# Kernel optimization log

Measured on AMD Instinct MI355X. Metric: run time of the kernel, lower is better.

The kernel has to match this reference:

```python
import jax, jax.numpy as jnp
import numpy as np


def setup_inputs() -> dict:
    key = jax.random.key(0)
    k1, k2, k3 = jax.random.split(key, 3)
    B, T, D = 64, 256, 512
    real = jax.random.normal(k1, (B, T, D), dtype=jnp.float32)
    imag = jax.random.normal(k2, (B, T, D), dtype=jnp.float32)
    weight = jax.random.uniform(k3, (B, T, 1), dtype=jnp.float32)
    return {"real": real, "imag": imag, "weight": weight}


def reference(real, imag, weight):
    # Weighted complex outer-product mixture:
    #   out_r[b] = sum_t w[b,t] * (r_t r_t^T + i_t i_t^T)
    #   out_i[b] = sum_t w[b,t] * (i_t r_t^T - r_t i_t^T)
    # Equivalent to the original per-sample loop + TxDxD outer products,
    # but fused: scale one operand by w and contract over t directly.
    w = weight[..., 0]  # [B, T]
    rw = real * w[..., None]  # [B, T, D]
    iw = imag * w[..., None]
    out_r = jnp.einsum('btd,bte->bde', rw, real) + jnp.einsum('btd,bte->bde', iw, imag)
    out_i = jnp.einsum('btd,bte->bde', iw, real) - jnp.einsum('btd,bte->bde', rw, imag)
    return (out_r, out_i)
```

## Files before the change

kernel.cpp:

```cpp
#include <hip/hip_runtime.h>
#include <cstdint>
#include <cstddef>

#define BB 64
#define TT 256
#define DD 512
#define BK 32
#define TILEM 128

typedef short bf16x8 __attribute__((ext_vector_type(8)));
typedef float f32x4  __attribute__((ext_vector_type(4)));

typedef __attribute__((address_space(1))) const void* gptr_t;
typedef __attribute__((address_space(3))) void* sptr_t;

static __device__ __forceinline__ unsigned short f2bf(float x) {
  unsigned u = __builtin_bit_cast(unsigned, x) + 0x8000u;
  return (unsigned short)(u >> 16);
}

__global__ __launch_bounds__(256, 2)
void ComplexMixture_54838142435828_kernel(const float* __restrict__ re,
                                          const float* __restrict__ im,
                                          const float* __restrict__ wt,
                                          float* __restrict__ out) {
  __shared__ __attribute__((aligned(16))) float sT[4 * BK * 128];
  __shared__ float sw[TT];

  const int tid = threadIdx.x;

  const int L = blockIdx.x;
  const int c = L & 7;
  const int s = L >> 3;
  const int b  = c * 8 + (s >> 4);
  const int t5 = s & 15;
  const int d0 = (t5 >> 2) * TILEM;
  const int e0 = (t5 & 3) * TILEM;

  sw[tid] = wt[b * TT + tid];

  const int lane = tid & 63;
  const int wid  = tid >> 6;
  const int wm = (wid >> 1) * 64;
  const int wn = (wid & 1) * 64;
  const int quad = lane >> 4;
  const int l16  = lane & 15;

  const int scol = (wid & 2) ? e0 : d0;
  const float* sbase = (wid & 1) ? im : re;
  const int ksub  = lane >> 5;
  const int dloc4 = (lane & 31) * 4;

  f32x4 accR[4][4], accI[4][4];
  #pragma unroll
  for (int mt = 0; mt < 4; ++mt)
    #pragma unroll
    for (int nt = 0; nt < 4; ++nt) {
      accR[mt][nt] = (f32x4){0.f, 0.f, 0.f, 0.f};
      accI[mt][nt] = (f32x4){0.f, 0.f, 0.f, 0.f};
    }

  for (int kt = 0; kt < TT; kt += BK) {
    __syncthreads();

    const float* gsrc = sbase + ((size_t)(b * TT + kt + ksub)) * DD + scol + dloc4;
    float* lbase = &sT[wid * (BK * 128)];
    #pragma unroll
    for (int p = 0; p < 16; ++p) {
      __builtin_amdgcn_global_load_lds((gptr_t)(const void*)(gsrc + (size_t)(2 * p) * DD),
                                       (sptr_t)(void*)(lbase + p * 256),
                                       16, 0, 0);
    }
    __syncthreads();

    float wv[8];
    #pragma unroll
    for (int j = 0; j < 8; ++j) wv[j] = sw[kt + quad * 8 + j];

    bf16x8 bR[4], bI[4];
    #pragma unroll
    for (int nt = 0; nt < 4; ++nt) {
      const int dl = wn + nt * 16 + l16;
      union { unsigned short h[8]; bf16x8 v; } ur, ui;
      #pragma unroll
      for (int j = 0; j < 8; ++j) {
        ur.h[j] = f2bf(sT[2 * (BK * 128) + (quad * 8 + j) * 128 + dl]);
        ui.h[j] = f2bf(sT[3 * (BK * 128) + (quad * 8 + j) * 128 + dl]);
      }
      bR[nt] = ur.v;
      bI[nt] = ui.v;
    }

    #pragma unroll
    for (int mt = 0; mt < 4; ++mt) {
      const int dl = wm + mt * 16 + l16;
      union { unsigned short h[8]; bf16x8 v; } ur, ui;
      #pragma unroll
      for (int j = 0; j < 8; ++j) {
        const float r = sT[0 * (BK * 128) + (quad * 8 + j) * 128 + dl] * wv[j];
        const float i = sT[1 * (BK * 128) + (quad * 8 + j) * 128 + dl] * wv[j];
        ur.h[j] = f2bf(r);
        ui.h[j] = f2bf(i);
      }
      const bf16x8 aR = ur.v;
      const bf16x8 aI = ui.v;
      const bf16x8 aRn = aR ^ (bf16x8)((short)0x8000);
      #pragma unroll
      for (int nt = 0; nt < 4; ++nt) {
        accR[mt][nt] = __builtin_amdgcn_mfma_f32_16x16x32_bf16(aR,  bR[nt], accR[mt][nt], 0, 0, 0);
        accR[mt][nt] = __builtin_amdgcn_mfma_f32_16x16x32_bf16(aI,  bI[nt], accR[mt][nt], 0, 0, 0);
        accI[mt][nt] = __builtin_amdgcn_mfma_f32_16x16x32_bf16(aI,  bR[nt], accI[mt][nt], 0, 0, 0);
        accI[mt][nt] = __builtin_amdgcn_mfma_f32_16x16x32_bf16(aRn, bI[nt], accI[mt][nt], 0, 0, 0);
      }
    }
  }

  const size_t NOFF = (size_t)BB * DD * DD;
  #pragma unroll
  for (int mt = 0; mt < 4; ++mt) {
    #pragma unroll
    for (int r = 0; r < 4; ++r) {
      const int drow = d0 + wm + mt * 16 + quad * 4 + r;
      const size_t rowOff = ((size_t)(b * DD + drow)) * DD;
      #pragma unroll
      for (int nt = 0; nt < 4; ++nt) {
        const int ecol = e0 + wn + nt * 16 + l16;
        out[rowOff + ecol]        = accR[mt][nt][r];
        out[NOFF + rowOff + ecol] = accI[mt][nt][r];
      }
    }
  }
}

extern "C" void kernel_launch(void* const* d_in, const int* in_sizes, int n_in,
                              void* d_out, int out_size, void* d_ws, size_t ws_size,
                              hipStream_t stream) {
  const float* re = (const float*)d_in[0];
  const float* im = (const float*)d_in[1];
  const float* wt = (const float*)d_in[2];
  float* out = (float*)d_out;
  ComplexMixture_54838142435828_kernel<<<dim3(1024), dim3(256), 0, stream>>>(re, im, wt, out);
}
```

Before: 225.8 us.

## Exploit Hermitian symmetry, switch to 32x32 MFMA and double-buffer LDS staging

Uses the symmetry out_r^T = out_r and out_i^T = -out_i to compute only the 10 upper-triangular 128x128 tiles per batch. Off-diagonal tiles write their mirror through an LDS transpose. Also switches to 32x32x16 bf16 MFMA with BK=16 and double-buffers the global-to-LDS staging so the next chunk loads while the current one computes. This removes roughly 37.5% of the MFMA and load work. In exchange it adds extra transposed stores, more syncs, and an uneven grid of 640 blocks.

```diff
diff --git a/kernel.cpp b/kernel.cpp
--- a/kernel.cpp
+++ b/kernel.cpp
@@ -5,11 +5,12 @@
 #define BB 64
 #define TT 256
 #define DD 512
-#define BK 32
+#define BK 16
 #define TILEM 128
 
 typedef short bf16x8 __attribute__((ext_vector_type(8)));
-typedef float f32x4  __attribute__((ext_vector_type(4)));
+typedef float f32x16 __attribute__((ext_vector_type(16)));
+typedef float f32x4v __attribute__((ext_vector_type(4)));
 
 typedef __attribute__((address_space(1))) const void* gptr_t;
 typedef __attribute__((address_space(3))) void* sptr_t;
@@ -19,23 +20,22 @@
   return (unsigned short)(u >> 16);
 }
 
+#define STG(buf, t, idx) sB[(buf) * 8192 + (t) * 2048 + (idx)]
+
 __global__ __launch_bounds__(256, 2)
 void ComplexMixture_54838142435828_kernel(const float* __restrict__ re,
                                           const float* __restrict__ im,
                                           const float* __restrict__ wt,
                                           float* __restrict__ out) {
-  __shared__ __attribute__((aligned(16))) float sT[4 * BK * 128];
+  __shared__ __attribute__((aligned(16))) float sB[16896];
   __shared__ float sw[TT];
 
   const int tid = threadIdx.x;
-
-  const int L = blockIdx.x;
-  const int c = L & 7;
-  const int s = L >> 3;
-  const int b  = c * 8 + (s >> 4);
-  const int t5 = s & 15;
-  const int d0 = (t5 >> 2) * TILEM;
-  const int e0 = (t5 & 3) * TILEM;
+  const int b = blockIdx.y;
+  static const int TIa[10] = {0, 1, 1, 2, 2, 2, 3, 3, 3, 3};
+  static const int TJa[10] = {0, 0, 1, 0, 1, 2, 0, 1, 2, 3};
+  const int d0 = TIa[blockIdx.x] * TILEM;
+  const int e0 = TJa[blockIdx.x] * TILEM;
 
   sw[tid] = wt[b * TT + tid];
 
@@ -43,90 +43,120 @@
   const int wid  = tid >> 6;
   const int wm = (wid >> 1) * 64;
   const int wn = (wid & 1) * 64;
-  const int quad = lane >> 4;
-  const int l16  = lane & 15;
+  const int kh  = lane >> 5;
+  const int l32 = lane & 31;
 
+  const float* sbase = (wid & 1) ? im : re;
   const int scol = (wid & 2) ? e0 : d0;
-  const float* sbase = (wid & 1) ? im : re;
-  const int ksub  = lane >> 5;
-  const int dloc4 = (lane & 31) * 4;
+  const int dl4  = l32 * 4;
 
-  f32x4 accR[4][4], accI[4][4];
+  f32x16 accR[2][2], accI[2][2];
   #pragma unroll
-  for (int mt = 0; mt < 4; ++mt)
+  for (int mt = 0; mt < 2; ++mt)
     #pragma unroll
-    for (int nt = 0; nt < 4; ++nt) {
-      accR[mt][nt] = (f32x4){0.f, 0.f, 0.f, 0.f};
-      accI[mt][nt] = (f32x4){0.f, 0.f, 0.f, 0.f};
+    for (int nt = 0; nt < 2; ++nt) {
+      #pragma unroll
+      for (int r = 0; r < 16; ++r) { accR[mt][nt][r] = 0.f; accI[mt][nt][r] = 0.f; }
     }
 
-  for (int kt = 0; kt < TT; kt += BK) {
+  auto stage = [&](int it, int buf) {
+    const float* g = sbase + ((size_t)(b * TT + it * BK + kh)) * DD + scol + dl4;
+    const int lb = buf * 8192 + wid * 2048;
+    #pragma unroll
+    for (int p = 0; p < 8; ++p) {
+      __builtin_amdgcn_global_load_lds((gptr_t)(const void*)(g + (size_t)(2 * p) * DD),
+                                       (sptr_t)(void*)&sB[lb + p * 256], 16, 0, 0);
+    }
+  };
+
+  stage(0, 0);
+
+  for (int it = 0; it < TT / BK; ++it) {
     __syncthreads();
-
-    const float* gsrc = sbase + ((size_t)(b * TT + kt + ksub)) * DD + scol + dloc4;
-    float* lbase = &sT[wid * (BK * 128)];
-    #pragma unroll
-    for (int p = 0; p < 16; ++p) {
-      __builtin_amdgcn_global_load_lds((gptr_t)(const void*)(gsrc + (size_t)(2 * p) * DD),
-                                       (sptr_t)(void*)(lbase + p * 256),
-                                       16, 0, 0);
-    }
-    __syncthreads();
+    if (it < TT / BK - 1) stage(it + 1, (it + 1) & 1);
+    const int buf = it & 1;
 
     float wv[8];
     #pragma unroll
-    for (int j = 0; j < 8; ++j) wv[j] = sw[kt + quad * 8 + j];
+    for (int j = 0; j < 8; ++j) wv[j] = sw[it * BK + kh * 8 + j];
 
-    bf16x8 bR[4], bI[4];
+    bf16x8 aR[2], aI[2], bR[2], bI[2];
     #pragma unroll
-    for (int nt = 0; nt < 4; ++nt) {
-      const int dl = wn + nt * 16 + l16;
+    for (int mt = 0; mt < 2; ++mt) {
+      const int m = wm + mt * 32 + l32;
       union { unsigned short h[8]; bf16x8 v; } ur, ui;
       #pragma unroll
       for (int j = 0; j < 8; ++j) {
-        ur.h[j] = f2bf(sT[2 * (BK * 128) + (quad * 8 + j) * 128 + dl]);
-        ui.h[j] = f2bf(sT[3 * (BK * 128) + (quad * 8 + j) * 128 + dl]);
+        const int idx = (kh * 8 + j) * 128 + m;
+        ur.h[j] = f2bf(STG(buf, 0, idx) * wv[j]);
+        ui.h[j] = f2bf(STG(buf, 1, idx) * wv[j]);
       }
-      bR[nt] = ur.v;
-      bI[nt] = ui.v;
+      aR[mt] = ur.v; aI[mt] = ui.v;
+    }
+    #pragma unroll
+    for (int nt = 0; nt < 2; ++nt) {
+      const int n = wn + nt * 32 + l32;
+      union { unsigned short h[8]; bf16x8 v; } ur, ui;
+      #pragma unroll
+      for (int j = 0; j < 8; ++j) {
+        const int idx = (kh * 8 + j) * 128 + n;
+        ur.h[j] = f2bf(STG(buf, 2, idx));
+        ui.h[j] = f2bf(STG(buf, 3, idx));
+      }
+      bR[nt] = ur.v; bI[nt] = ui.v;
     }
 
     #pragma unroll
-    for (int mt = 0; mt < 4; ++mt) {
-      const int dl = wm + mt * 16 + l16;
-      union { unsigned short h[8]; bf16x8 v; } ur, ui;
+    for (int mt = 0; mt < 2; ++mt) {
+      const bf16x8 aRn = aR[mt] ^ (bf16x8)((short)0x8000);
       #pragma unroll
-      for (int j = 0; j < 8; ++j) {
-        const float r = sT[0 * (BK * 128) + (quad * 8 + j) * 128 + dl] * wv[j];
-        const float i = sT[1 * (BK * 128) + (quad * 8 + j) * 128 + dl] * wv[j];
-        ur.h[j] = f2bf(r);
-        ui.h[j] = f2bf(i);
-      }
-      const bf16x8 aR = ur.v;
-      const bf16x8 aI = ui.v;
-      const bf16x8 aRn = aR ^ (bf16x8)((short)0x8000);
-      #pragma unroll
-      for (int nt = 0; nt < 4; ++nt) {
-        accR[mt][nt] = __builtin_amdgcn_mfma_f32_16x16x32_bf16(aR,  bR[nt], accR[mt][nt], 0, 0, 0);
-        accR[mt][nt] = __builtin_amdgcn_mfma_f32_16x16x32_bf16(aI,  bI[nt], accR[mt][nt], 0, 0, 0);
-        accI[mt][nt] = __builtin_amdgcn_mfma_f32_16x16x32_bf16(aI,  bR[nt], accI[mt][nt], 0, 0, 0);
-        accI[mt][nt] = __builtin_amdgcn_mfma_f32_16x16x32_bf16(aRn, bI[nt], accI[mt][nt], 0, 0, 0);
+      for (int nt = 0; nt < 2; ++nt) {
+        accR[mt][nt] = __builtin_amdgcn_mfma_f32_32x32x16_bf16(aR[mt], bR[nt], accR[mt][nt], 0, 0, 0);
+        accR[mt][nt] = __builtin_amdgcn_mfma_f32_32x32x16_bf16(aI[mt], bI[nt], accR[mt][nt], 0, 0, 0);
+        accI[mt][nt] = __builtin_amdgcn_mfma_f32_32x32x16_bf16(aI[mt], bR[nt], accI[mt][nt], 0, 0, 0);
+        accI[mt][nt] = __builtin_amdgcn_mfma_f32_32x32x16_bf16(aRn,    bI[nt], accI[mt][nt], 0, 0, 0);
       }
     }
   }
 
   const size_t NOFF = (size_t)BB * DD * DD;
   #pragma unroll
-  for (int mt = 0; mt < 4; ++mt) {
+  for (int mt = 0; mt < 2; ++mt) {
     #pragma unroll
-    for (int r = 0; r < 4; ++r) {
-      const int drow = d0 + wm + mt * 16 + quad * 4 + r;
-      const size_t rowOff = ((size_t)(b * DD + drow)) * DD;
+    for (int r = 0; r < 16; ++r) {
+      const int row_l = (r & 3) + 8 * (r >> 2) + 4 * kh;
+      const size_t rowOff = ((size_t)(b * DD + d0 + wm + mt * 32 + row_l)) * DD;
       #pragma unroll
-      for (int nt = 0; nt < 4; ++nt) {
-        const int ecol = e0 + wn + nt * 16 + l16;
-        out[rowOff + ecol]        = accR[mt][nt][r];
-        out[NOFF + rowOff + ecol] = accI[mt][nt][r];
+      for (int nt = 0; nt < 2; ++nt) {
+        const int col = e0 + wn + nt * 32 + l32;
+        out[rowOff + col]        = accR[mt][nt][r];
+        out[NOFF + rowOff + col] = accI[mt][nt][r];
+      }
+    }
+  }
+
+  if (d0 != e0) {
+    #pragma unroll
+    for (int pass = 0; pass < 2; ++pass) {
+      __syncthreads();
+      #pragma unroll
+      for (int mt = 0; mt < 2; ++mt)
+        #pragma unroll
+        for (int nt = 0; nt < 2; ++nt)
+          #pragma unroll
+          for (int r = 0; r < 16; ++r) {
+            const int rr = wm + mt * 32 + (r & 3) + 8 * (r >> 2) + 4 * kh;
+            const int cc = wn + nt * 32 + l32;
+            sB[cc * 132 + rr] = pass == 0 ? accR[mt][nt][r] : -accI[mt][nt][r];
+          }
+      __syncthreads();
+      const size_t base = (pass == 0 ? (size_t)0 : NOFF) + (size_t)b * DD * DD;
+      #pragma unroll 4
+      for (int q = 0; q < 16; ++q) {
+        const int c  = q * 8 + (tid >> 5);
+        const int r4 = (tid & 31) * 4;
+        f32x4v v = *(const f32x4v*)&sB[c * 132 + r4];
+        *(f32x4v*)&out[base + (size_t)(e0 + c) * DD + d0 + r4] = v;
       }
     }
   }
@@ -139,5 +169,5 @@
   const float* im = (const float*)d_in[1];
   const float* wt = (const float*)d_in[2];
   float* out = (float*)d_out;
-  ComplexMixture_54838142435828_kernel<<<dim3(1024), dim3(256), 0, stream>>>(re, im, wt, out);
+  ComplexMixture_54838142435828_kernel<<<dim3(10, BB), dim3(256), 0, stream>>>(re, im, wt, out);
 }
```

Result: faster. 220.7 us (-2.3%).
